# Kernel tuning notes

Hardware: AMD Instinct MI355X
Metric: run time of the kernel (lower is better)

The kernel has to match this reference:

```python
import jax, jax.numpy as jnp
import numpy as np

B, C, H, W = 8, 192, 256, 256

def setup_inputs() -> dict:
    key = jax.random.key(0)
    k1, k2, k3, k4, k5 = jax.random.split(key, 5)
    x = jax.random.normal(k1, (B, C, H, W), dtype=jnp.float32)
    w1 = jax.random.normal(k2, (C, 1, 1, 1), dtype=jnp.float32) * 0.1
    w3 = jax.random.normal(k3, (C, 1, 3, 3), dtype=jnp.float32) * 0.1
    w5 = jax.random.normal(k4, (C, 1, 5, 5), dtype=jnp.float32) * 0.1
    alpha = jax.random.normal(k5, (4,), dtype=jnp.float32)
    return {"x": x, "w1": w1, "w3": w3, "w5": w5, "alpha": alpha}

def _dwconv(x, w, pad):
    # depthwise conv: feature_group_count == channels, kernel (C,1,k,k)
    return jax.lax.conv_general_dilated(
        x, w, window_strides=(1, 1), padding=[(pad, pad), (pad, pad)],
        dimension_numbers=("NCHW", "OIHW", "NCHW"),
        feature_group_count=x.shape[1])

def reference(x, w1, w3, w5, alpha):
    out1 = _dwconv(x, w1, 0)
    out3 = _dwconv(x, w3, 1)
    out5 = _dwconv(x, w5, 2)
    return alpha[0] * x + alpha[1] * out1 + alpha[2] * out3 + alpha[3] * out5
```

## Files before the change

kernel.cpp:

```cpp
#include <hip/hip_runtime.h>


typedef float f32x4 __attribute__((ext_vector_type(4)));

constexpr int Bn = 8, Cn = 192, Hn = 256, Wn = 256;
constexpr int HALF    = 128;
constexpr int PH      = 16;
constexpr int NPH     = HALF / PH;
constexpr int SLOTS   = 32;
constexpr int LSTRIDE = 260;

__global__ __launch_bounds__(256)
void omnishift_kernel(const float* __restrict__ x,
                      const float* __restrict__ w1,
                      const float* __restrict__ w3,
                      const float* __restrict__ w5,
                      const float* __restrict__ alpha,
                      float* __restrict__ out)
{
    __shared__ float lds[SLOTS * LSTRIDE];

    const int tid   = threadIdx.x;
    const int wg    = blockIdx.x;
    const int plane = wg >> 1;
    const int half  = wg & 1;
    const int r0    = half * HALF;
    const int c     = plane % Cn;

    const float a0 = alpha[0], a1 = alpha[1], a2 = alpha[2], a3 = alpha[3];
    float wf[5][5];
#pragma unroll
    for (int i = 0; i < 5; ++i)
#pragma unroll
        for (int j = 0; j < 5; ++j) {
            float v = a3 * w5[(c * 5 + i) * 5 + j];
            if (i >= 1 && i <= 3 && j >= 1 && j <= 3)
                v += a2 * w3[(c * 3 + (i - 1)) * 3 + (j - 1)];
            if (i == 2 && j == 2)
                v += a1 * w1[c] + a0;
            wf[i][j] = v;
        }

    const float* xp = x   + (size_t)plane * (Hn * Wn);
    float*       op = out + (size_t)plane * (Hn * Wn);

    if (tid < SLOTS * 4) {
        const int r   = tid >> 2;
        const int q   = tid & 3;
        const int col = (q < 2) ? q : (256 + q);
        lds[r * LSTRIDE + col] = 0.f;
    }

#pragma unroll
    for (int i = 0; i < 5; ++i) {
        const int fidx = tid + i * 256;
        const int row  = fidx >> 6;
        const int l    = fidx & 63;
        const int gr   = r0 + row - 2;
        float4 v = make_float4(0.f, 0.f, 0.f, 0.f);
        if ((unsigned)gr < (unsigned)Hn)
            v = *reinterpret_cast<const float4*>(xp + gr * Wn + 4 * l);
        float* dst = &lds[row * LSTRIDE + 2 + 4 * l];
        *reinterpret_cast<float2*>(dst)     = make_float2(v.x, v.y);
        *reinterpret_cast<float2*>(dst + 2) = make_float2(v.z, v.w);
    }
    __syncthreads();

    const int ct  = tid & 63;
    const int rg  = tid >> 6;
    const int oc0 = 4 * ct;

    auto phase = [&](const int p, const int sbase) {
        float4 st[4];
        if (p < NPH - 1) {
#pragma unroll
            for (int i = 0; i < 4; ++i) {
                const int fidx = tid + i * 256;
                const int row  = fidx >> 6;
                const int l    = fidx & 63;
                const int gr   = r0 + PH * p + 18 + row;
                st[i] = make_float4(0.f, 0.f, 0.f, 0.f);
                if (gr < Hn)
                    st[i] = *reinterpret_cast<const float4*>(xp + gr * Wn + 4 * l);
            }
        }

        float win[5][8];
#pragma unroll
        for (int i = 0; i < 4; ++i) {
            const int slot = (sbase + 4 * rg + i) & (SLOTS - 1);
            const float* src = &lds[slot * LSTRIDE + oc0];
#pragma unroll
            for (int j = 0; j < 8; ++j) win[i][j] = src[j];
        }

        f32x4 o[4];
#pragma unroll
        for (int k = 0; k < 4; ++k) {
            const int slot = (sbase + 4 * rg + 4 + k) & (SLOTS - 1);
            const float* src = &lds[slot * LSTRIDE + oc0];
#pragma unroll
            for (int j = 0; j < 8; ++j) win[4][j] = src[j];

#pragma unroll
            for (int jj = 0; jj < 4; ++jj) {
                float acc = 0.f;
#pragma unroll
                for (int i = 0; i < 5; ++i)
#pragma unroll
                    for (int d = 0; d < 5; ++d)
                        acc += win[i][jj + d] * wf[i][d];
                o[k][jj] = acc;
            }
#pragma unroll
            for (int i = 0; i < 4; ++i)
#pragma unroll
                for (int j = 0; j < 8; ++j) win[i][j] = win[i + 1][j];
        }

        if (p < NPH - 1) {
            asm volatile("s_waitcnt lgkmcnt(0)\n\ts_barrier" ::: "memory");
#pragma unroll
            for (int i = 0; i < 4; ++i) {
                const int fidx = tid + i * 256;
                const int row  = fidx >> 6;
                const int l    = fidx & 63;
                const int slot = (sbase + 20 + row) & (SLOTS - 1);
                float* dst = &lds[slot * LSTRIDE + 2 + 4 * l];
                *reinterpret_cast<float2*>(dst)     = make_float2(st[i].x, st[i].y);
                *reinterpret_cast<float2*>(dst + 2) = make_float2(st[i].z, st[i].w);
            }
        }

        float* outp = op + (size_t)(r0 + PH * p + 4 * rg) * Wn + oc0;
#pragma unroll
        for (int k = 0; k < 4; ++k)
            *reinterpret_cast<f32x4*>(outp + (size_t)k * Wn) = o[k];

        if (p < NPH - 1) {
            asm volatile("s_waitcnt lgkmcnt(0)\n\ts_barrier" ::: "memory");
        }
    };

#pragma unroll 1
    for (int pp = 0; pp < NPH / 2; ++pp) {
        phase(2 * pp,     0);
        phase(2 * pp + 1, 16);
    }
}

extern "C" void kernel_launch(void* const* d_in, const int* in_sizes, int n_in,
                              void* d_out, int out_size, void* d_ws, size_t ws_size,
                              hipStream_t stream)
{
    const float* x     = (const float*)d_in[0];
    const float* w1    = (const float*)d_in[1];
    const float* w3    = (const float*)d_in[2];
    const float* w5    = (const float*)d_in[3];
    const float* alpha = (const float*)d_in[4];
    float* out = (float*)d_out;

    omnishift_kernel<<<Bn * Cn * 2, 256, 0, stream>>>(x, w1, w3, w5, alpha, out);
}
```

Baseline: 156.6 us.

## Split planes into 64-row bands, process three bands per block with smaller LDS ring

Each plane is now split into four 64-row bands instead of two halves. Every block handles three consecutive bands in a persistent loop, using a 16-slot LDS ring and 8-row phases in which each thread computes two output rows. Filter weights are forced into scalar registers with readfirstlane, and launch bounds ask for higher occupancy. The aim is more blocks resident per CU and fewer registers, at the cost of reloading halo rows for each band and a trailing barrier after the final phase.

```diff
diff --git a/kernel.cpp b/kernel.cpp
--- a/kernel.cpp
+++ b/kernel.cpp
@@ -4,13 +4,20 @@
 typedef float f32x4 __attribute__((ext_vector_type(4)));
 
 constexpr int Bn = 8, Cn = 192, Hn = 256, Wn = 256;
-constexpr int HALF    = 128;
-constexpr int PH      = 16;
-constexpr int NPH     = HALF / PH;
-constexpr int SLOTS   = 32;
+constexpr int BAND    = 64;
+constexpr int PH      = 8;
+constexpr int NPH     = BAND / PH;
+constexpr int SLOTS   = 16;
 constexpr int LSTRIDE = 260;
+constexpr int NBANDS  = Bn * Cn * (Hn / BAND);
+constexpr int NBLK    = NBANDS / 3;
 
-__global__ __launch_bounds__(256)
+__device__ __forceinline__ float uniformf(float v) {
+    return __builtin_bit_cast(float,
+        __builtin_amdgcn_readfirstlane(__builtin_bit_cast(int, v)));
+}
+
+__global__ __launch_bounds__(256, 8)
 void omnishift_kernel(const float* __restrict__ x,
                       const float* __restrict__ w1,
                       const float* __restrict__ w3,
@@ -20,29 +27,9 @@
 {
     __shared__ float lds[SLOTS * LSTRIDE];
 
-    const int tid   = threadIdx.x;
-    const int wg    = blockIdx.x;
-    const int plane = wg >> 1;
-    const int half  = wg & 1;
-    const int r0    = half * HALF;
-    const int c     = plane % Cn;
-
-    const float a0 = alpha[0], a1 = alpha[1], a2 = alpha[2], a3 = alpha[3];
-    float wf[5][5];
-#pragma unroll
-    for (int i = 0; i < 5; ++i)
-#pragma unroll
-        for (int j = 0; j < 5; ++j) {
-            float v = a3 * w5[(c * 5 + i) * 5 + j];
-            if (i >= 1 && i <= 3 && j >= 1 && j <= 3)
-                v += a2 * w3[(c * 3 + (i - 1)) * 3 + (j - 1)];
-            if (i == 2 && j == 2)
-                v += a1 * w1[c] + a0;
-            wf[i][j] = v;
-        }
-
-    const float* xp = x   + (size_t)plane * (Hn * Wn);
-    float*       op = out + (size_t)plane * (Hn * Wn);
+    const int tid = threadIdx.x;
+    const int ct  = tid & 63;
+    const int rg  = tid >> 6;
 
     if (tid < SLOTS * 4) {
         const int r   = tid >> 2;
@@ -51,101 +38,102 @@
         lds[r * LSTRIDE + col] = 0.f;
     }
 
+#pragma unroll 1
+    for (int ib = 0; ib < 3; ++ib) {
+        const int w     = blockIdx.x * 3 + ib;
+        const int plane = w >> 2;
+        const int band  = w & 3;
+        const int r0    = band * BAND;
+        const int c     = plane % Cn;
+
+        const float a0 = alpha[0], a1 = alpha[1], a2 = alpha[2], a3 = alpha[3];
+        float wfs[5][5];
 #pragma unroll
-    for (int i = 0; i < 5; ++i) {
-        const int fidx = tid + i * 256;
-        const int row  = fidx >> 6;
-        const int l    = fidx & 63;
-        const int gr   = r0 + row - 2;
-        float4 v = make_float4(0.f, 0.f, 0.f, 0.f);
-        if ((unsigned)gr < (unsigned)Hn)
-            v = *reinterpret_cast<const float4*>(xp + gr * Wn + 4 * l);
-        float* dst = &lds[row * LSTRIDE + 2 + 4 * l];
-        *reinterpret_cast<float2*>(dst)     = make_float2(v.x, v.y);
-        *reinterpret_cast<float2*>(dst + 2) = make_float2(v.z, v.w);
-    }
-    __syncthreads();
+        for (int i = 0; i < 5; ++i)
+#pragma unroll
+            for (int j = 0; j < 5; ++j) {
+                float v = a3 * w5[(c * 5 + i) * 5 + j];
+                if (i >= 1 && i <= 3 && j >= 1 && j <= 3)
+                    v += a2 * w3[(c * 3 + (i - 1)) * 3 + (j - 1)];
+                if (i == 2 && j == 2)
+                    v += a1 * w1[c] + a0;
+                wfs[i][j] = uniformf(v);
+            }
 
-    const int ct  = tid & 63;
-    const int rg  = tid >> 6;
-    const int oc0 = 4 * ct;
-
-    auto phase = [&](const int p, const int sbase) {
-        float4 st[4];
-        if (p < NPH - 1) {
-#pragma unroll
-            for (int i = 0; i < 4; ++i) {
-                const int fidx = tid + i * 256;
-                const int row  = fidx >> 6;
-                const int l    = fidx & 63;
-                const int gr   = r0 + PH * p + 18 + row;
-                st[i] = make_float4(0.f, 0.f, 0.f, 0.f);
-                if (gr < Hn)
-                    st[i] = *reinterpret_cast<const float4*>(xp + gr * Wn + 4 * l);
-            }
-        }
-
-        float win[5][8];
-#pragma unroll
-        for (int i = 0; i < 4; ++i) {
-            const int slot = (sbase + 4 * rg + i) & (SLOTS - 1);
-            const float* src = &lds[slot * LSTRIDE + oc0];
-#pragma unroll
-            for (int j = 0; j < 8; ++j) win[i][j] = src[j];
-        }
-
-        f32x4 o[4];
-#pragma unroll
-        for (int k = 0; k < 4; ++k) {
-            const int slot = (sbase + 4 * rg + 4 + k) & (SLOTS - 1);
-            const float* src = &lds[slot * LSTRIDE + oc0];
-#pragma unroll
-            for (int j = 0; j < 8; ++j) win[4][j] = src[j];
+        const float* xp = x   + (size_t)plane * (Hn * Wn);
+        float*       op = out + (size_t)plane * (Hn * Wn);
 
 #pragma unroll
-            for (int jj = 0; jj < 4; ++jj) {
-                float acc = 0.f;
+        for (int i = 0; i < 3; ++i) {
+            const int idx = tid + i * 256;
+            const int row = idx >> 6;
+            const int l   = idx & 63;
+            const int gr  = r0 + row - 2;
+            f32x4 v = {0.f, 0.f, 0.f, 0.f};
+            if ((unsigned)gr < (unsigned)Hn)
+                v = *reinterpret_cast<const f32x4*>(xp + (size_t)gr * Wn + 4 * l);
+            float* dst = &lds[row * LSTRIDE + 2 + 4 * l];
+            dst[0] = v.x; dst[1] = v.y; dst[2] = v.z; dst[3] = v.w;
+        }
+        __syncthreads();
+
+        auto phase = [&](const int p, const int sbase) {
+            f32x4 st0 = {0.f,0.f,0.f,0.f}, st1 = {0.f,0.f,0.f,0.f};
+            if (p < NPH - 1) {
+                const int gr0 = r0 + PH * p + 10 + rg;
+                const int gr1 = gr0 + 4;
+                if (gr0 < Hn) st0 = *reinterpret_cast<const f32x4*>(xp + (size_t)gr0 * Wn + 4 * ct);
+                if (gr1 < Hn) st1 = *reinterpret_cast<const f32x4*>(xp + (size_t)gr1 * Wn + 4 * ct);
+            }
+
+            f32x4 accA = {0.f,0.f,0.f,0.f}, accB = {0.f,0.f,0.f,0.f};
 #pragma unroll
-                for (int i = 0; i < 5; ++i)
+            for (int off = 0; off < 6; ++off) {
+                const int slot = (sbase + 2 * rg + off) & (SLOTS - 1);
+                const float* src = &lds[slot * LSTRIDE + 4 * ct];
+                float rw[8];
+#pragma unroll
+                for (int j = 0; j < 8; ++j) rw[j] = src[j];
+                if (off <= 4) {
 #pragma unroll
                     for (int d = 0; d < 5; ++d)
-                        acc += win[i][jj + d] * wf[i][d];
-                o[k][jj] = acc;
+#pragma unroll
+                        for (int j = 0; j < 4; ++j)
+                            accA[j] += rw[j + d] * wfs[off][d];
+                }
+                if (off >= 1) {
+#pragma unroll
+                    for (int d = 0; d < 5; ++d)
+#pragma unroll
+                        for (int j = 0; j < 4; ++j)
+                            accB[j] += rw[j + d] * wfs[off - 1][d];
+                }
             }
-#pragma unroll
-            for (int i = 0; i < 4; ++i)
-#pragma unroll
-                for (int j = 0; j < 8; ++j) win[i][j] = win[i + 1][j];
-        }
 
-        if (p < NPH - 1) {
             asm volatile("s_waitcnt lgkmcnt(0)\n\ts_barrier" ::: "memory");
-#pragma unroll
-            for (int i = 0; i < 4; ++i) {
-                const int fidx = tid + i * 256;
-                const int row  = fidx >> 6;
-                const int l    = fidx & 63;
-                const int slot = (sbase + 20 + row) & (SLOTS - 1);
-                float* dst = &lds[slot * LSTRIDE + 2 + 4 * l];
-                *reinterpret_cast<float2*>(dst)     = make_float2(st[i].x, st[i].y);
-                *reinterpret_cast<float2*>(dst + 2) = make_float2(st[i].z, st[i].w);
+
+            if (p < NPH - 1) {
+                const int s0 = (sbase + 12 + rg) & (SLOTS - 1);
+                const int s1 = (sbase + 12 + rg + 4) & (SLOTS - 1);
+                float* d0 = &lds[s0 * LSTRIDE + 2 + 4 * ct];
+                float* d1 = &lds[s1 * LSTRIDE + 2 + 4 * ct];
+                d0[0] = st0.x; d0[1] = st0.y; d0[2] = st0.z; d0[3] = st0.w;
+                d1[0] = st1.x; d1[1] = st1.y; d1[2] = st1.z; d1[3] = st1.w;
             }
-        }
 
-        float* outp = op + (size_t)(r0 + PH * p + 4 * rg) * Wn + oc0;
-#pragma unroll
-        for (int k = 0; k < 4; ++k)
-            *reinterpret_cast<f32x4*>(outp + (size_t)k * Wn) = o[k];
+            float* outp = op + (size_t)(r0 + PH * p + 2 * rg) * Wn + 4 * ct;
+            *reinterpret_cast<f32x4*>(outp)      = accA;
+            *reinterpret_cast<f32x4*>(outp + Wn) = accB;
 
-        if (p < NPH - 1) {
-            asm volatile("s_waitcnt lgkmcnt(0)\n\ts_barrier" ::: "memory");
-        }
-    };
+            if (p < NPH - 1)
+                asm volatile("s_waitcnt lgkmcnt(0)\n\ts_barrier" ::: "memory");
+        };
 
 #pragma unroll 1
-    for (int pp = 0; pp < NPH / 2; ++pp) {
-        phase(2 * pp,     0);
-        phase(2 * pp + 1, 16);
+        for (int pp = 0; pp < NPH / 2; ++pp) {
+            phase(2 * pp,     0);
+            phase(2 * pp + 1, 8);
+        }
     }
 }
 
@@ -160,5 +148,5 @@
     const float* alpha = (const float*)d_in[4];
     float* out = (float*)d_out;
 
-    omnishift_kernel<<<Bn * Cn * 2, 256, 0, stream>>>(x, w1, w3, w5, alpha, out);
+    omnishift_kernel<<<NBLK, 256, 0, stream>>>(x, w1, w3, w5, alpha, out);
 }
```

Measured after the change: 225.5 us. 44.0% more time.
